# Performance work log

Hardware: AMD Instinct MI355X
Metric: run time of the kernel (lower is better)

## Reference

```python
import jax, jax.numpy as jnp
from jax import lax
import numpy as np

B, C_IN, C_OUT, H, W = 4, 256, 256, 4, 8192
HD = C_OUT // H          # head_dim = 64
K_ATT = 7
PAD = (1 * (K_ATT - 1) + 1) // 2  # = 3 (dilation=1)
CK = 1                   # conv_kernel_size (must be 1 for the module's shapes to be consistent)


def setup_inputs() -> dict:
    key = jax.random.key(0)
    ks = jax.random.split(key, 14)
    s = 0.05
    inp = {
        "x": jax.random.normal(ks[0], (B, C_IN, W), dtype=jnp.float32),
        # 1x1 convs q/k/v: weight [C_out, C_in], bias [C_out]
        "w1": jax.random.normal(ks[1], (C_OUT, C_IN), dtype=jnp.float32) * (C_IN ** -0.5),
        "b1": jax.random.normal(ks[2], (C_OUT,), dtype=jnp.float32) * s,
        "w2": jax.random.normal(ks[3], (C_OUT, C_IN), dtype=jnp.float32) * (C_IN ** -0.5),
        "b2": jax.random.normal(ks[4], (C_OUT,), dtype=jnp.float32) * s,
        "w3": jax.random.normal(ks[5], (C_OUT, C_IN), dtype=jnp.float32) * (C_IN ** -0.5),
        "b3": jax.random.normal(ks[6], (C_OUT,), dtype=jnp.float32) * s,
        # conv_p: Conv1d(1, head_dim, 1): weight [HD], bias [HD]
        "wp": jax.random.normal(ks[7], (HD,), dtype=jnp.float32) * s,
        "bp": jax.random.normal(ks[8], (HD,), dtype=jnp.float32) * s,
        # fc: Conv2d(3*H, CK, 1, bias=False): weight [CK, 3H]
        "fc_w": jax.random.normal(ks[9], (CK, 3 * H), dtype=jnp.float32) * ((3 * H) ** -0.5),
        # dep_conv: Conv1d(CK*HD -> C_OUT, kernel=CK, groups=HD): weight [C_OUT, CK, CK], bias [C_OUT]
        "dep_w": jax.random.normal(ks[10], (C_OUT, CK, CK), dtype=jnp.float32) * s,
        "dep_b": jax.random.normal(ks[11], (C_OUT,), dtype=jnp.float32) * s,
        "rate1": jnp.float32(0.5),
        "rate2": jnp.float32(0.5),
    }
    return inp


def _conv1x1(x, w, b):  # x: [B, Cin, W] -> [B, Cout, W]
    return jnp.einsum('oc,bcw->bow', w, x) + b[None, :, None]


def _unfold(p):  # p: [..., Wp] -> windows [..., W, K_ATT]
    idx = jnp.arange(W)[:, None] + jnp.arange(K_ATT)[None, :]
    return p[..., idx]


def _forward(x, w1, b1, w2, b2, w3, b3, wp, bp, fc_w, dep_w, dep_b, rate1, rate2):
    q = _conv1x1(x, w1, b1)   # [B, C, W]
    k = _conv1x1(x, w2, b2)
    v = _conv1x1(x, w3, b3)
    scaling = HD ** -0.5

    # positional encoding: conv_p(linspace(-1,1,W)) -> [HD, W]
    loc = jnp.linspace(-1.0, 1.0, W, dtype=jnp.float32)
    pe = wp[:, None] * loc[None, :] + bp[:, None]

    q_att = q.reshape(B * H, HD, W) * scaling
    k_att = k.reshape(B * H, HD, W)
    v_att = v.reshape(B * H, HD, W)

    # reflection pad last axis by PAD, then unfold to [.., HD, W, K]
    pad3 = lambda t: jnp.pad(t, ((0, 0), (0, 0), (PAD, PAD)), mode='reflect')
    uk = _unfold(pad3(k_att))                                   # [BH, HD, W, K]
    uv = _unfold(pad3(v_att))                                   # [BH, HD, W, K]
    upe = _unfold(jnp.pad(pe, ((0, 0), (PAD, PAD)), mode='reflect'))  # [HD, W, K]

    # att = sum_d q * (unfold_k + q_pe - unfold_rpe); softmax over window K
    D = pe[:, :, None] - upe                                     # [HD, W, K]
    att = jnp.einsum('bdw,bdwk->bwk', q_att, uk + D[None])       # [BH, W, K]
    att = jax.nn.softmax(att, axis=-1)
    out_att = jnp.einsum('bwk,bdwk->bdw', att, uv).reshape(B, C_OUT, W)

    # conv branch: fc over concatenated heads, then grouped dep_conv
    qkv = jnp.concatenate([q.reshape(B, H, HD, W),
                           k.reshape(B, H, HD, W),
                           v.reshape(B, H, HD, W)], axis=1)      # [B, 3H, HD, W]
    f_all = jnp.einsum('oc,bcdw->bodw', fc_w, qkv)               # [B, CK, HD, W]
    f_conv = jnp.transpose(f_all, (0, 2, 1, 3)).reshape(B, HD * CK, W)
    out_conv = lax.conv_general_dilated(
        f_conv, dep_w, window_strides=(1,), padding='VALID',
        dimension_numbers=('NCH', 'OIH', 'NCH'), feature_group_count=HD)
    out_conv = out_conv + dep_b[None, :, None]

    return rate1 * out_att + rate2 * out_conv


def reference(x, w1, b1, w2, b2, w3, b3, wp, bp, fc_w, dep_w, dep_b, rate1, rate2):
    return _forward(x, w1, b1, w2, b2, w3, b3, wp, bp, fc_w, dep_w, dep_b, rate1, rate2)
```

## Files before the change

### kernel.cpp

```cpp
#include <hip/hip_runtime.h>
#include <stdint.h>
#include <stddef.h>

typedef unsigned short u16;
typedef unsigned int   u32;

typedef __attribute__((ext_vector_type(8))) short bf16x8;
typedef __attribute__((ext_vector_type(4))) float f32x4;

__device__ __forceinline__ float b2f_lo(u32 v) { return __uint_as_float(v << 16); }
__device__ __forceinline__ float b2f_hi(u32 v) { return __uint_as_float(v & 0xFFFF0000u); }
__device__ __forceinline__ u16 f2b(float f){
  u32 x = __float_as_uint(f);
  return (u16)((x + 0x7FFFu + ((x >> 16) & 1u)) >> 16);
}
__device__ __forceinline__ int refl(int w){ return w < 0 ? -w : (w > 8191 ? 16382 - w : w); }
__device__ __forceinline__ void up8(const uint4 v, float* f){
  f[0] = b2f_lo(v.x); f[1] = b2f_hi(v.x); f[2] = b2f_lo(v.y); f[3] = b2f_hi(v.y);
  f[4] = b2f_lo(v.z); f[5] = b2f_hi(v.z); f[6] = b2f_lo(v.w); f[7] = b2f_hi(v.w);
}

__global__ __launch_bounds__(256) void k_build(const float* __restrict__ w1, const float* __restrict__ b1,
                                               const float* __restrict__ w2, const float* __restrict__ b2,
                                               const float* __restrict__ w3, const float* __restrict__ b3,
                                               const float* __restrict__ fcw,
                                               u16* __restrict__ Wall, float* __restrict__ ball){
  const int r = blockIdx.x, c = threadIdx.x;
  float v = 0.f, bv = 0.f;
  if (r < 256){      v = w1[(r << 8) + c];          bv = b1[r]; }
  else if (r < 512){ v = w2[((r - 256) << 8) + c];  bv = b2[r - 256]; }
  else if (r < 768){ v = w3[((r - 512) << 8) + c];  bv = b3[r - 512]; }
  else if (r < 832){
    const int d = r - 768;
    float s = 0.f, sbias = 0.f;
#pragma unroll
    for (int h = 0; h < 4; ++h){
      const int ch = (h << 6) + d;
      const float f1 = fcw[h], f2 = fcw[4 + h], f3 = fcw[8 + h];
      s     += f1 * w1[(ch << 8) + c] + f2 * w2[(ch << 8) + c] + f3 * w3[(ch << 8) + c];
      sbias += f1 * b1[ch] + f2 * b2[ch] + f3 * b3[ch];
    }
    v = s; bv = sbias;
  }
  Wall[(r << 8) + c] = f2b(v);
  if (c == 0) ball[r] = bv;
}

__global__ __launch_bounds__(256, 1) void fused_acmix(
    const u16* __restrict__ Wall, const float* __restrict__ ball,
    const float* __restrict__ x, const float* __restrict__ wp,
    const float* __restrict__ depw, const float* __restrict__ depb,
    const float* __restrict__ r1p, const float* __restrict__ r2p,
    float* __restrict__ out)
{
  __shared__ __align__(16) u16 Bl [80 * 256];
  __shared__ __align__(16) u16 As [128 * 64];
  __shared__ __align__(16) u16 Ql [64 * 256];
  __shared__ __align__(16) u16 KVl[70 * 512];
  __shared__ float wpL[64];
  u16* Fl = As;

  const int bid = blockIdx.x;
  const int w_id = ((bid & 7) << 6) + (bid >> 3);
  const int b = w_id >> 7;
  const int stripe = w_id & 127;
  const int w0 = stripe << 6;

  const int t = threadIdx.x;
  const int wv = t >> 6, lane = t & 63;
  const int quad = lane >> 4, l15 = lane & 15;

  if (t < 64) wpL[t] = wp[t];

  {
    const float* xb = x + ((size_t)b << 21);
    const int cg = wv;
    const int rl = lane;
#pragma unroll
    for (int ci = 0; ci < 8; ++ci){
      const int cc = cg + (ci << 2);
#pragma unroll
      for (int rb = 0; rb < 2; ++rb){
        const int r = rl + (rb << 6);
        if (r < 80){
          const int w = refl(w0 - 4 + r);
          u32 pk0, pk1, pk2, pk3;
          {
            const size_t base = ((size_t)(cc << 3)) << 13;
            const float f0 = xb[base + (0u << 13) + w];
            const float f1 = xb[base + (1u << 13) + w];
            const float f2 = xb[base + (2u << 13) + w];
            const float f3 = xb[base + (3u << 13) + w];
            const float f4 = xb[base + (4u << 13) + w];
            const float f5 = xb[base + (5u << 13) + w];
            const float f6 = xb[base + (6u << 13) + w];
            const float f7 = xb[base + (7u << 13) + w];
            pk0 = (u32)f2b(f0) | ((u32)f2b(f1) << 16);
            pk1 = (u32)f2b(f2) | ((u32)f2b(f3) << 16);
            pk2 = (u32)f2b(f4) | ((u32)f2b(f5) << 16);
            pk3 = (u32)f2b(f6) | ((u32)f2b(f7) << 16);
          }
          *(uint4*)((char*)Bl + r * 512 + ((cc ^ (r & 31)) << 4)) = make_uint4(pk0, pk1, pk2, pk3);
        }
      }
    }
  }

  uint4 ra[4];
  auto loadA = [&](int mt_, int kc_){
#pragma unroll
    for (int k4 = 0; k4 < 4; ++k4){
      const int task = t + (k4 << 8);
      const int row = task >> 3, u = task & 7;
      ra[k4] = *(const uint4*)(Wall + (((mt_ << 7) + row) << 8) + (kc_ << 6) + (u << 3));
    }
  };
  loadA(0, 0);

#pragma unroll
  for (int mt = 0; mt < 7; ++mt){
    f32x4 acc[2][5] = {};
#pragma unroll
    for (int kc = 0; kc < 4; ++kc){
      __syncthreads();
#pragma unroll
      for (int k4 = 0; k4 < 4; ++k4){
        const int task = t + (k4 << 8);
        const int row = task >> 3, u = (task & 7) ^ (row & 7);
        *(uint4*)((char*)As + row * 128 + (u << 4)) = ra[k4];
      }
      __syncthreads();
      {
        const int idx = (mt << 2) + kc;
        if (idx < 27) loadA((idx + 1) >> 2, (idx + 1) & 3);
      }
#pragma unroll
      for (int ks = 0; ks < 2; ++ks){
        bf16x8 av[2], bv[5];
#pragma unroll
        for (int i = 0; i < 2; ++i){
          const int rowA = (wv << 5) + (i << 4) + l15;
          const int ca = ((ks << 2) + quad) ^ (rowA & 7);
          av[i] = *(const bf16x8*)((const char*)As + rowA * 128 + (ca << 4));
        }
#pragma unroll
        for (int j = 0; j < 5; ++j){
          const int rowB = (j << 4) + l15;
          const int cb = ((kc << 3) + (ks << 2) + quad) ^ (rowB & 31);
          bv[j] = *(const bf16x8*)((const char*)Bl + rowB * 512 + (cb << 4));
        }
#pragma unroll
        for (int i = 0; i < 2; ++i)
#pragma unroll
          for (int j = 0; j < 5; ++j)
            acc[i][j] = __builtin_amdgcn_mfma_f32_16x16x32_bf16(av[i], bv[j], acc[i][j], 0, 0, 0);
      }
    }

    if (mt == 6) __syncthreads();
#pragma unroll
    for (int i = 0; i < 2; ++i){
      const int mloc = (wv << 5) + (i << 4) + (quad << 2);
      const float4 bias = *(const float4*)(ball + (mt << 7) + mloc);
#pragma unroll
      for (int j = 0; j < 5; ++j){
        const int r = (j << 4) + l15;
        f32x4 c = acc[i][j];
        uint2 val;
        val.x = (u32)f2b(c.x + bias.x) | ((u32)f2b(c.y + bias.y) << 16);
        val.y = (u32)f2b(c.z + bias.z) | ((u32)f2b(c.w + bias.w) << 16);
        if (mt < 2){
          const int wl = r - 4;
          if ((unsigned)wl < 64u){
            const int chunk = ((mt << 7) + mloc) >> 3;
            *(uint2*)((char*)Ql + wl * 512 + ((chunk ^ (wl & 31)) << 4) + ((quad & 1) << 3)) = val;
          }
        } else if (mt < 6){
          const int rr = r - 1;
          if ((unsigned)rr < 70u){
            const int chunk = (((mt - 2) << 7) + mloc) >> 3;
            *(uint2*)((char*)KVl + rr * 1024 + ((chunk ^ (rr & 31)) << 4) + ((quad & 1) << 3)) = val;
          }
        } else {
          const int wl = r - 4;
          if ((unsigned)wl < 64u && mloc < 64){
            const int chunk = mloc >> 3;
            *(uint2*)((char*)Fl + wl * 128 + ((chunk ^ (wl & 7)) << 4) + ((quad & 1) << 3)) = val;
          }
        }
      }
    }
  }
  __syncthreads();

  const int h = t >> 6, wl = t & 63;
  const int w = w0 + wl;

  float att[7] = {0.f,0.f,0.f,0.f,0.f,0.f,0.f};
  float qd = 0.f;
#pragma unroll
  for (int e = 0; e < 8; ++e){
    const int cq = (h << 3) + e;
    const uint4 q4 = *(const uint4*)((const char*)Ql + wl * 512 + ((cq ^ (wl & 31)) << 4));
    float qf[8]; up8(q4, qf);
#pragma unroll
    for (int d = 0; d < 8; ++d) qd += qf[d] * wpL[(e << 3) + d];
#pragma unroll
    for (int kk = 0; kk < 7; ++kk){
      const int rr = wl + kk;
      const uint4 k4 = *(const uint4*)((const char*)KVl + rr * 1024 + ((((h << 3) + e) ^ (rr & 31)) << 4));
      float kf[8]; up8(k4, kf);
      att[kk] += qf[0]*kf[0] + qf[1]*kf[1] + qf[2]*kf[2] + qf[3]*kf[3]
               + qf[4]*kf[4] + qf[5]*kf[5] + qf[6]*kf[6] + qf[7]*kf[7];
    }
  }

  const float locw = -1.f + (2.f / 8191.f) * (float)w;
  float mx = -1e30f;
#pragma unroll
  for (int kk = 0; kk < 7; ++kk){
    const int wr = refl(w + kk - 3);
    const float lr = -1.f + (2.f / 8191.f) * (float)wr;
    att[kk] = 0.125f * (att[kk] + (locw - lr) * qd);
    mx = fmaxf(mx, att[kk]);
  }
  float p[7]; float ssum = 0.f;
#pragma unroll
  for (int kk = 0; kk < 7; ++kk){ p[kk] = __expf(att[kk] - mx); ssum += p[kk]; }
  const float inv = 1.f / ssum;
#pragma unroll
  for (int kk = 0; kk < 7; ++kk) p[kk] *= inv;

  float fvv[16];
  {
    const int c0 = h << 1;
    const uint4 f0 = *(const uint4*)((const char*)Fl + wl * 128 + ((c0 ^ (wl & 7)) << 4));
    const uint4 f1 = *(const uint4*)((const char*)Fl + wl * 128 + (((c0 + 1) ^ (wl & 7)) << 4));
    up8(f0, fvv); up8(f1, fvv + 8);
  }

  const float r1 = r1p[0];
  const float r2 = r2p[0];

#pragma unroll
  for (int e = 0; e < 8; ++e){
    float o8[8] = {0.f,0.f,0.f,0.f,0.f,0.f,0.f,0.f};
#pragma unroll
    for (int kk = 0; kk < 7; ++kk){
      const int rr = wl + kk;
      const uint4 v4 = *(const uint4*)((const char*)KVl + rr * 1024 + (((32 + (h << 3) + e) ^ (rr & 31)) << 4));
      float vf[8]; up8(v4, vf);
      const float pk = p[kk];
      o8[0] += pk * vf[0]; o8[1] += pk * vf[1]; o8[2] += pk * vf[2]; o8[3] += pk * vf[3];
      o8[4] += pk * vf[4]; o8[5] += pk * vf[5]; o8[6] += pk * vf[6]; o8[7] += pk * vf[7];
    }
#pragma unroll
    for (int s = 0; s < 8; ++s){
      const int dl = (e << 3) + s;
      const float oc = depw[(h << 6) + dl] * fvv[dl >> 2] + depb[(h << 6) + dl];
      out[(((size_t)((b << 8) + (h << 6) + dl)) << 13) + w] = r1 * o8[s] + r2 * oc;
    }
  }
}

extern "C" void kernel_launch(void* const* d_in, const int* in_sizes, int n_in,
                              void* d_out, int out_size, void* d_ws, size_t ws_size,
                              hipStream_t stream){
  (void)in_sizes; (void)n_in; (void)out_size; (void)ws_size;
  const float* x    = (const float*)d_in[0];
  const float* w1   = (const float*)d_in[1];
  const float* b1   = (const float*)d_in[2];
  const float* w2   = (const float*)d_in[3];
  const float* b2   = (const float*)d_in[4];
  const float* w3   = (const float*)d_in[5];
  const float* b3   = (const float*)d_in[6];
  const float* wp   = (const float*)d_in[7];
  const float* fcw  = (const float*)d_in[9];
  const float* depw = (const float*)d_in[10];
  const float* depb = (const float*)d_in[11];
  const float* r1p  = (const float*)d_in[12];
  const float* r2p  = (const float*)d_in[13];
  float* out = (float*)d_out;

  char* ws = (char*)d_ws;
  u16*   Wall = (u16*)(ws);
  float* ball = (float*)(ws + 458752);

  k_build<<<dim3(896, 1, 1), 256, 0, stream>>>(w1, b1, w2, b2, w3, b3, fcw, Wall, ball);
  fused_acmix<<<dim3(512, 1, 1), 256, 0, stream>>>(Wall, ball, x, wp, depw, depb, r1p, r2p, out);
}
```

Before: 214.7 us.

## Widen fused kernel to 1024 threads and split GEMM and attention across waves

The fused block grows from 4 to 16 waves. Each wave now owns a 32-row M tile of the weight GEMM and reads its A fragments straight from global memory, which drops the LDS-staged A double buffer and its barriers. The attention phase splits each (head, position) across 4 lanes with shuffle reductions, and the conv branch reads only its slice of F. This aims to hide more latency through higher wave count, at the cost of uncached global A reads and output stores that are less contiguous per wavefront.

```diff
diff --git a/kernel.cpp b/kernel.cpp
--- a/kernel.cpp
+++ b/kernel.cpp
@@ -46,7 +46,7 @@
   if (c == 0) ball[r] = bv;
 }
 
-__global__ __launch_bounds__(256, 1) void fused_acmix(
+__global__ __launch_bounds__(1024, 1) void fused_acmix(
     const u16* __restrict__ Wall, const float* __restrict__ ball,
     const float* __restrict__ x, const float* __restrict__ wp,
     const float* __restrict__ depw, const float* __restrict__ depb,
@@ -54,94 +54,54 @@
     float* __restrict__ out)
 {
   __shared__ __align__(16) u16 Bl [80 * 256];
-  __shared__ __align__(16) u16 As [128 * 64];
   __shared__ __align__(16) u16 Ql [64 * 256];
   __shared__ __align__(16) u16 KVl[70 * 512];
+  __shared__ __align__(16) u16 Fl [64 * 64];
   __shared__ float wpL[64];
-  u16* Fl = As;
 
   const int bid = blockIdx.x;
   const int w_id = ((bid & 7) << 6) + (bid >> 3);
   const int b = w_id >> 7;
-  const int stripe = w_id & 127;
-  const int w0 = stripe << 6;
+  const int w0 = (w_id & 127) << 6;
 
   const int t = threadIdx.x;
-  const int wv = t >> 6, lane = t & 63;
+  const int wave = t >> 6, lane = t & 63;
   const int quad = lane >> 4, l15 = lane & 15;
 
   if (t < 64) wpL[t] = wp[t];
 
   {
     const float* xb = x + ((size_t)b << 21);
-    const int cg = wv;
-    const int rl = lane;
-#pragma unroll
-    for (int ci = 0; ci < 8; ++ci){
-      const int cc = cg + (ci << 2);
-#pragma unroll
-      for (int rb = 0; rb < 2; ++rb){
-        const int r = rl + (rb << 6);
-        if (r < 80){
-          const int w = refl(w0 - 4 + r);
-          u32 pk0, pk1, pk2, pk3;
-          {
-            const size_t base = ((size_t)(cc << 3)) << 13;
-            const float f0 = xb[base + (0u << 13) + w];
-            const float f1 = xb[base + (1u << 13) + w];
-            const float f2 = xb[base + (2u << 13) + w];
-            const float f3 = xb[base + (3u << 13) + w];
-            const float f4 = xb[base + (4u << 13) + w];
-            const float f5 = xb[base + (5u << 13) + w];
-            const float f6 = xb[base + (6u << 13) + w];
-            const float f7 = xb[base + (7u << 13) + w];
-            pk0 = (u32)f2b(f0) | ((u32)f2b(f1) << 16);
-            pk1 = (u32)f2b(f2) | ((u32)f2b(f3) << 16);
-            pk2 = (u32)f2b(f4) | ((u32)f2b(f5) << 16);
-            pk3 = (u32)f2b(f6) | ((u32)f2b(f7) << 16);
-          }
-          *(uint4*)((char*)Bl + r * 512 + ((cc ^ (r & 31)) << 4)) = make_uint4(pk0, pk1, pk2, pk3);
-        }
+    for (int idx = t; idx < 2560; idx += 1024){
+      const int cc = idx / 80;
+      const int r  = idx - cc * 80;
+      const int w  = refl(w0 - 4 + r);
+      const float* px = xb + (((size_t)cc) << 16) + w;
+      u32 pk[4];
+#pragma unroll
+      for (int jj = 0; jj < 4; ++jj){
+        const float f0 = px[(size_t)(2 * jj)     << 13];
+        const float f1 = px[(size_t)(2 * jj + 1) << 13];
+        pk[jj] = (u32)f2b(f0) | ((u32)f2b(f1) << 16);
       }
-    }
-  }
-
-  uint4 ra[4];
-  auto loadA = [&](int mt_, int kc_){
-#pragma unroll
-    for (int k4 = 0; k4 < 4; ++k4){
-      const int task = t + (k4 << 8);
-      const int row = task >> 3, u = task & 7;
-      ra[k4] = *(const uint4*)(Wall + (((mt_ << 7) + row) << 8) + (kc_ << 6) + (u << 3));
-    }
-  };
-  loadA(0, 0);
-
-#pragma unroll
-  for (int mt = 0; mt < 7; ++mt){
+      *(uint4*)((char*)Bl + r * 512 + ((cc ^ (r & 31)) << 4)) = make_uint4(pk[0], pk[1], pk[2], pk[3]);
+    }
+  }
+  __syncthreads();
+
+  for (int qt = wave; qt < 26; qt += 16){
+    const int mt = qt >> 2, mq = qt & 3;
+    const int mbase = (mt << 7) + (mq << 5);
     f32x4 acc[2][5] = {};
 #pragma unroll
     for (int kc = 0; kc < 4; ++kc){
-      __syncthreads();
-#pragma unroll
-      for (int k4 = 0; k4 < 4; ++k4){
-        const int task = t + (k4 << 8);
-        const int row = task >> 3, u = (task & 7) ^ (row & 7);
-        *(uint4*)((char*)As + row * 128 + (u << 4)) = ra[k4];
-      }
-      __syncthreads();
-      {
-        const int idx = (mt << 2) + kc;
-        if (idx < 27) loadA((idx + 1) >> 2, (idx + 1) & 3);
-      }
 #pragma unroll
       for (int ks = 0; ks < 2; ++ks){
         bf16x8 av[2], bv[5];
 #pragma unroll
         for (int i = 0; i < 2; ++i){
-          const int rowA = (wv << 5) + (i << 4) + l15;
-          const int ca = ((ks << 2) + quad) ^ (rowA & 7);
-          av[i] = *(const bf16x8*)((const char*)As + rowA * 128 + (ca << 4));
+          const int row = mbase + (i << 4) + l15;
+          av[i] = *(const bf16x8*)(Wall + (row << 8) + (kc << 6) + (ks << 5) + (quad << 3));
         }
 #pragma unroll
         for (int j = 0; j < 5; ++j){
@@ -156,11 +116,9 @@
             acc[i][j] = __builtin_amdgcn_mfma_f32_16x16x32_bf16(av[i], bv[j], acc[i][j], 0, 0, 0);
       }
     }
-
-    if (mt == 6) __syncthreads();
 #pragma unroll
     for (int i = 0; i < 2; ++i){
-      const int mloc = (wv << 5) + (i << 4) + (quad << 2);
+      const int mloc = (mq << 5) + (i << 4) + (quad << 2);
       const float4 bias = *(const float4*)(ball + (mt << 7) + mloc);
 #pragma unroll
       for (int j = 0; j < 5; ++j){
@@ -183,7 +141,7 @@
           }
         } else {
           const int wl = r - 4;
-          if ((unsigned)wl < 64u && mloc < 64){
+          if ((unsigned)wl < 64u){
             const int chunk = mloc >> 3;
             *(uint2*)((char*)Fl + wl * 128 + ((chunk ^ (wl & 7)) << 4) + ((quad & 1) << 3)) = val;
           }
@@ -193,13 +151,16 @@
   }
   __syncthreads();
 
-  const int h = t >> 6, wl = t & 63;
+  const int es = t & 3;
+  const int q_ = t >> 2;
+  const int h = q_ >> 6, wl = q_ & 63;
   const int w = w0 + wl;
 
   float att[7] = {0.f,0.f,0.f,0.f,0.f,0.f,0.f};
   float qd = 0.f;
 #pragma unroll
-  for (int e = 0; e < 8; ++e){
+  for (int ee = 0; ee < 2; ++ee){
+    const int e = (es << 1) + ee;
     const int cq = (h << 3) + e;
     const uint4 q4 = *(const uint4*)((const char*)Ql + wl * 512 + ((cq ^ (wl & 31)) << 4));
     float qf[8]; up8(q4, qf);
@@ -208,12 +169,19 @@
 #pragma unroll
     for (int kk = 0; kk < 7; ++kk){
       const int rr = wl + kk;
-      const uint4 k4 = *(const uint4*)((const char*)KVl + rr * 1024 + ((((h << 3) + e) ^ (rr & 31)) << 4));
+      const uint4 k4 = *(const uint4*)((const char*)KVl + rr * 1024 + ((cq ^ (rr & 31)) << 4));
       float kf[8]; up8(k4, kf);
       att[kk] += qf[0]*kf[0] + qf[1]*kf[1] + qf[2]*kf[2] + qf[3]*kf[3]
                + qf[4]*kf[4] + qf[5]*kf[5] + qf[6]*kf[6] + qf[7]*kf[7];
     }
   }
+#pragma unroll
+  for (int kk = 0; kk < 7; ++kk){
+    att[kk] += __shfl_xor(att[kk], 1);
+    att[kk] += __shfl_xor(att[kk], 2);
+  }
+  qd += __shfl_xor(qd, 1);
+  qd += __shfl_xor(qd, 2);
 
   const float locw = -1.f + (2.f / 8191.f) * (float)w;
   float mx = -1e30f;
@@ -231,19 +199,19 @@
 #pragma unroll
   for (int kk = 0; kk < 7; ++kk) p[kk] *= inv;
 
-  float fvv[16];
+  float fq[4];
   {
-    const int c0 = h << 1;
-    const uint4 f0 = *(const uint4*)((const char*)Fl + wl * 128 + ((c0 ^ (wl & 7)) << 4));
-    const uint4 f1 = *(const uint4*)((const char*)Fl + wl * 128 + (((c0 + 1) ^ (wl & 7)) << 4));
-    up8(f0, fvv); up8(f1, fvv + 8);
-  }
-
+    const int cf = (h << 1) + (es >> 1);
+    const uint2 fb = *(const uint2*)((const char*)Fl + wl * 128 + ((cf ^ (wl & 7)) << 4) + ((es & 1) << 3));
+    fq[0] = b2f_lo(fb.x); fq[1] = b2f_hi(fb.x);
+    fq[2] = b2f_lo(fb.y); fq[3] = b2f_hi(fb.y);
+  }
   const float r1 = r1p[0];
   const float r2 = r2p[0];
 
 #pragma unroll
-  for (int e = 0; e < 8; ++e){
+  for (int ee = 0; ee < 2; ++ee){
+    const int e = (es << 1) + ee;
     float o8[8] = {0.f,0.f,0.f,0.f,0.f,0.f,0.f,0.f};
 #pragma unroll
     for (int kk = 0; kk < 7; ++kk){
@@ -257,7 +225,7 @@
 #pragma unroll
     for (int s = 0; s < 8; ++s){
       const int dl = (e << 3) + s;
-      const float oc = depw[(h << 6) + dl] * fvv[dl >> 2] + depb[(h << 6) + dl];
+      const float oc = depw[(h << 6) + dl] * fq[(ee << 1) + (s >> 2)] + depb[(h << 6) + dl];
       out[(((size_t)((b << 8) + (h << 6) + dl)) << 13) + w] = r1 * o8[s] + r2 * oc;
     }
   }
@@ -287,5 +255,5 @@
   float* ball = (float*)(ws + 458752);
 
   k_build<<<dim3(896, 1, 1), 256, 0, stream>>>(w1, b1, w2, b2, w3, b3, fcw, Wall, ball);
-  fused_acmix<<<dim3(512, 1, 1), 256, 0, stream>>>(Wall, ball, x, wp, depw, depb, r1p, r2p, out);
-}
+  fused_acmix<<<dim3(512, 1, 1), 1024, 0, stream>>>(Wall, ball, x, wp, depw, depb, r1p, r2p, out);
+}
```

Result: slower. 255.4 us (+19.0%).
